# Performance work log

Hardware: AMD Instinct MI355X
Metric: run time of the kernel (lower is better)

## Reference

```python
import jax, jax.numpy as jnp
import numpy as np
import math

EMBED_DIM = 512
NUM_HEADS = 8
NUM_EXPERTS = 16
TOP_K = 8
B, T = 2, 1024


def setup_inputs() -> dict:
    key = jax.random.key(0)
    ks = jax.random.split(key, 16)
    d, E = EMBED_DIM, NUM_EXPERTS
    hdim = 4 * d  # expert hidden width
    s = 0.02
    inp = {
        "x": jax.random.normal(ks[0], (B, T, d), jnp.float32),
        # RMSNorm params (init ones, matching torch module)
        "g": jnp.ones((d,), jnp.float32),
        "b": jnp.ones((d,), jnp.float32),
        # attention
        "c_attn_w": jax.random.normal(ks[1], (d, 3 * d), jnp.float32) * s,
        "c_attn_b": jnp.zeros((3 * d,), jnp.float32),
        "alpha": jnp.ones((NUM_HEADS,), jnp.float32),
        "c_proj_w": jax.random.normal(ks[2], (d, d), jnp.float32) * s,
        "c_proj_b": jnp.zeros((d,), jnp.float32),
        # router
        "router_w": jax.random.normal(ks[3], (d, E), jnp.float32) * s,
        "router_b": jnp.zeros((E,), jnp.float32),
        # stacked expert params: Linear(d,4d) -> SwiGLU(4d,4d) -> Linear(4d,d)
        "w_in": jax.random.normal(ks[4], (E, d, hdim), jnp.float32) * s,
        "b_in": jnp.zeros((E, hdim), jnp.float32),
        "w1": jax.random.normal(ks[5], (E, hdim, 2 * hdim), jnp.float32) * s,
        "b1": jnp.zeros((E, 2 * hdim), jnp.float32),
        "w2": jax.random.normal(ks[6], (E, hdim, hdim), jnp.float32) * s,
        "b2": jnp.zeros((E, hdim), jnp.float32),
        "w_out": jax.random.normal(ks[7], (E, hdim, d), jnp.float32) * s,
        "b_out": jnp.zeros((E, d), jnp.float32),
    }
    return inp


def _block(x, g, b, c_attn_w, c_attn_b, alpha, c_proj_w, c_proj_b,
           router_w, router_b, w_in, b_in, w1, b1, w2, b2, w_out, b_out):
    Bb, Tt, C = x.shape
    H = alpha.shape[0]
    hd = C // H
    E = router_b.shape[0]

    # RMSNorm (note: additive b, per original module)
    rms = jnp.sqrt(jnp.mean(x * x, axis=-1, keepdims=True) + 1e-6)
    xn = (x / rms) * g + b

    # QK-normalized causal attention
    qkv = xn @ c_attn_w + c_attn_b                      # [B,T,3C]
    q, k, v = jnp.split(qkv, 3, axis=-1)
    def heads(t):
        return t.reshape(Bb, Tt, H, hd).transpose(0, 2, 1, 3)  # [B,H,T,hd]
    q, k, v = heads(q), heads(k), heads(v)
    eps = 1e-5
    q_hat = q / (jnp.linalg.norm(q, axis=-1, keepdims=True) + eps)
    k_hat = k / (jnp.linalg.norm(k, axis=-1, keepdims=True) + eps)
    factor = (alpha * math.sqrt(hd)).reshape(1, H, 1, 1)
    q_scaled = q_hat * factor
    # SDPA default scale = 1/sqrt(head_dim)
    scores = jnp.einsum("bhqd,bhkd->bhqk", q_scaled, k_hat) / math.sqrt(hd)
    causal = jnp.tril(jnp.ones((Tt, Tt), bool))
    scores = jnp.where(causal, scores, -jnp.inf)
    att = jax.nn.softmax(scores, axis=-1)
    y = jnp.einsum("bhqk,bhkd->bhqd", att, v)
    y = y.transpose(0, 2, 1, 3).reshape(Bb, Tt, C)
    y = y @ c_proj_w + c_proj_b
    x = x + y

    # Router + top-8 normalized gates
    routes = jax.nn.softmax(x @ router_w + router_b, axis=-1)  # [B,T,E]
    probs, idx = jax.lax.top_k(routes, TOP_K)
    probs = probs / jnp.sum(probs, axis=-1, keepdims=True)
    # combine weights per expert: [B,T,E]
    gates = jnp.sum(jax.nn.one_hot(idx, E, dtype=x.dtype) * probs[..., None], axis=2)

    # Dense expert evaluation (faithful math: unselected tokens get zero gate)
    N = Bb * Tt
    xf = x.reshape(N, C)
    gf = gates.reshape(N, E)
    h = jnp.einsum("nd,edf->enf", xf, w_in) + b_in[:, None, :]      # [E,N,4d]
    c = jnp.einsum("enf,efg->eng", h, w1) + b1[:, None, :]          # [E,N,8d]
    a, bb2 = jnp.split(c, 2, axis=-1)
    s = (bb2 * jax.nn.sigmoid(bb2)) * a                              # SwiGLU
    o = jnp.einsum("enf,efg->eng", s, w2) + b2[:, None, :]          # [E,N,4d]
    eo = jnp.einsum("enf,efd->end", o, w_out) + b_out[:, None, :]   # [E,N,d]
    moe = jnp.einsum("end,ne->nd", eo, gf).reshape(Bb, Tt, C)
    return x + moe


def reference(x, g, b, c_attn_w, c_attn_b, alpha, c_proj_w, c_proj_b,
              router_w, router_b, w_in, b_in, w1, b1, w2, b2, w_out, b_out):
    return _block(x, g, b, c_attn_w, c_attn_b, alpha, c_proj_w, c_proj_b,
                  router_w, router_b, w_in, b_in, w1, b1, w2, b2, w_out, b_out)
```

## Files before the change

kernel.cpp:

```cpp
#include <hip/hip_runtime.h>
#include <stdint.h>

#define DEVI __device__ __forceinline__
#define FENCE() asm volatile("" ::: "memory")

typedef short short8 __attribute__((ext_vector_type(8)));
typedef short short4v __attribute__((ext_vector_type(4)));
typedef float f32x4 __attribute__((ext_vector_type(4)));

DEVI float bf2f(unsigned short s){ union{unsigned u; float f;} x; x.u = ((unsigned)s)<<16; return x.f; }
DEVI unsigned short f2bf(float f){ union{float f; unsigned u;} x; x.f=f; unsigned r = x.u + 0x7fff + ((x.u>>16)&1); return (unsigned short)(r>>16); }

DEVI void gload_lds16(const void* g, void* l){
  __builtin_amdgcn_global_load_lds((const __attribute__((address_space(1))) unsigned int*)g,
                                   (__attribute__((address_space(3))) unsigned int*)l, 16, 0, 0);
}

__global__ __launch_bounds__(256)
void transpose_cvt(const float* __restrict__ in, unsigned short* __restrict__ out, int K, int N)
{
  __shared__ float tile[32][33];
  size_t zoff = (size_t)blockIdx.z * K * N;
  const float* src = in + zoff;
  unsigned short* dst = out + zoff;
  int kb = blockIdx.y*32, nb = blockIdx.x*32;
  int t = threadIdx.x;
  int tr = t>>3, tc = (t&7)*4;
  float4 v = *(const float4*)(src + (size_t)(kb+tr)*N + nb + tc);
  tile[tr][tc+0]=v.x; tile[tr][tc+1]=v.y; tile[tr][tc+2]=v.z; tile[tr][tc+3]=v.w;
  __syncthreads();
  short4v ov;
  ov[0] = (short)f2bf(tile[tc+0][tr]);
  ov[1] = (short)f2bf(tile[tc+1][tr]);
  ov[2] = (short)f2bf(tile[tc+2][tr]);
  ov[3] = (short)f2bf(tile[tc+3][tr]);
  *(short4v*)(dst + (size_t)(nb+tr)*K + kb + tc) = ov;
}

__global__ __launch_bounds__(256)
void transpose_cvt_w1(const float* __restrict__ w1, unsigned short* __restrict__ outp)
{
  __shared__ float tile[32][33];
  int e = blockIdx.z;
  const float* src = w1 + (size_t)e*2048*4096;
  unsigned short* dst = outp + (size_t)e*4096*2048;
  int np0 = blockIdx.x*32;
  int k0 = blockIdx.y*32;
  int g = np0 >> 5;
  int t = threadIdx.x;
  int tr = t>>3, tc = (t&7)*4;
  int srccol = (tc < 16) ? (g*16 + tc) : (2048 + g*16 + (tc-16));
  float4 v = *(const float4*)(src + (size_t)(k0+tr)*4096 + srccol);
  tile[tr][tc+0]=v.x; tile[tr][tc+1]=v.y; tile[tr][tc+2]=v.z; tile[tr][tc+3]=v.w;
  __syncthreads();
  short4v ov;
  ov[0] = (short)f2bf(tile[tc+0][tr]);
  ov[1] = (short)f2bf(tile[tc+1][tr]);
  ov[2] = (short)f2bf(tile[tc+2][tr]);
  ov[3] = (short)f2bf(tile[tc+3][tr]);
  *(short4v*)(dst + (size_t)(np0+tr)*2048 + k0 + tc) = ov;
}

__global__ __launch_bounds__(256)
void rmsnorm_k(const float* __restrict__ x, const float* __restrict__ gw,
               const float* __restrict__ bw, unsigned short* __restrict__ xn)
{
  int row = blockIdx.x*4 + (threadIdx.x>>6);
  int lane = threadIdx.x & 63;
  const float* xr = x + (size_t)row*512 + lane*8;
  float4 a = *(const float4*)xr;
  float4 c = *(const float4*)(xr+4);
  float ss = a.x*a.x+a.y*a.y+a.z*a.z+a.w*a.w + c.x*c.x+c.y*c.y+c.z*c.z+c.w*c.w;
  #pragma unroll
  for (int m=1;m<64;m<<=1) ss += __shfl_xor(ss, m);
  float inv = 1.0f / sqrtf(ss*(1.f/512.f) + 1e-6f);
  const float* gr = gw + lane*8; const float* br = bw + lane*8;
  float4 g0=*(const float4*)gr, g1=*(const float4*)(gr+4);
  float4 b0=*(const float4*)br, b1=*(const float4*)(br+4);
  short8 o;
  o[0]=(short)f2bf(a.x*inv*g0.x + b0.x);
  o[1]=(short)f2bf(a.y*inv*g0.y + b0.y);
  o[2]=(short)f2bf(a.z*inv*g0.z + b0.z);
  o[3]=(short)f2bf(a.w*inv*g0.w + b0.w);
  o[4]=(short)f2bf(c.x*inv*g1.x + b1.x);
  o[5]=(short)f2bf(c.y*inv*g1.y + b1.y);
  o[6]=(short)f2bf(c.z*inv*g1.z + b1.z);
  o[7]=(short)f2bf(c.w*inv*g1.w + b1.w);
  *(short8*)(xn + (size_t)row*512 + lane*8) = o;
}

template<int EPI>
__global__ __launch_bounds__(512, 2)
void gemm3(const unsigned short* __restrict__ A, const unsigned short* __restrict__ B,
           const float* __restrict__ bias,
           float* __restrict__ Cf, unsigned short* __restrict__ Ch,
           int M, int N, int K,
           const int* __restrict__ off, long long strideBz, long long strideBiasz)
{
  __shared__ char smem[147456];
  int nbx = gridDim.x, nby = gridDim.y;
  int pl = nbx*nby;
  int lin = ((int)blockIdx.z*nby + (int)blockIdx.y)*nbx + (int)blockIdx.x;
  int nwg = pl*(int)gridDim.z;
  int cpx = nwg >> 3;
  int swz = (lin & 7)*cpx + (lin >> 3);
  int z  = swz / pl; int rxy = swz - z*pl;
  int by = rxy / nbx; int bx = rxy - by*nbx;

  int rowbase = 0, Mz = M;
  if (off){ rowbase = off[z]; Mz = off[z+1] - rowbase; }
  int row0 = by * 256;
  if (row0 >= Mz) return;
  int col0 = bx * 128;
  const unsigned short* Ab = A + (size_t)(rowbase + row0) * K;
  const unsigned short* Bb = B + (size_t)z * strideBz + (size_t)col0 * K;
  const float* biasz = bias + (size_t)z * strideBiasz;

  int tid = threadIdx.x;
  int lane = tid & 63, w = tid >> 6;
  int lrow = lane & 15, lg = lane >> 4;
  int wr = w >> 1, wc = w & 1;

  f32x4 acc[4][4];
  #pragma unroll
  for (int i=0;i<4;i++){
    #pragma unroll
    for (int j=0;j<4;j++) acc[i][j] = f32x4{0.f,0.f,0.f,0.f};
  }

  int nkt = K >> 6;

  auto stage = [&](int kt2, int part){
    if (kt2 >= nkt) return;
    char* sA = smem + (kt2 % 3) * 49152;
    char* sB = sA + 32768;
    int k0 = kt2 << 6;
    #pragma unroll
    for (int i=0;i<2;i++){
      int s = (part*2 + i)*512 + tid;
      int r = s >> 3, kb = (s & 7) ^ (r & 7);
      gload_lds16(Ab + (size_t)r*K + k0 + kb*8, sA + s*16);
    }
    {
      int s = part*512 + tid;
      int r = s >> 3, kb = (s & 7) ^ (r & 7);
      gload_lds16(Bb + (size_t)r*K + k0 + kb*8, sB + s*16);
    }
  };

  stage(0,0); stage(0,1); stage(1,0); stage(1,1);
  asm volatile("s_waitcnt vmcnt(6)" ::: "memory");
  __builtin_amdgcn_s_barrier();
  FENCE();

  for (int kt = 0; kt < nkt; kt++){
    char* sA = smem + (kt % 3) * 49152;
    char* sB = sA + 32768;
    short8 bfr[4][2], afr[4][2];
    #pragma unroll
    for (int n=0;n<4;n++){
      int ct = wc*64 + n*16 + lrow;
      #pragma unroll
      for (int kk=0;kk<2;kk++){
        int kbb = lg + kk*4;
        bfr[n][kk] = *(const short8*)(sB + ct*128 + ((kbb ^ (ct&7))<<4));
      }
    }
    #pragma unroll
    for (int m=0;m<2;m++){
      int rt = wr*64 + m*16 + lrow;
      #pragma unroll
      for (int kk=0;kk<2;kk++){
        int kbb = lg + kk*4;
        afr[m][kk] = *(const short8*)(sA + rt*128 + ((kbb ^ (rt&7))<<4));
      }
    }
    stage(kt+2, 0);
    FENCE(); __builtin_amdgcn_s_barrier(); FENCE();
    __builtin_amdgcn_s_setprio(1);
    #pragma unroll
    for (int m=0;m<2;m++){
      #pragma unroll
      for (int n=0;n<4;n++){
        #pragma unroll
        for (int kk=0;kk<2;kk++)
          acc[m][n] = __builtin_amdgcn_mfma_f32_16x16x32_bf16(afr[m][kk], bfr[n][kk], acc[m][n], 0,0,0);
      }
    }
    __builtin_amdgcn_s_setprio(0);
    FENCE(); __builtin_amdgcn_s_barrier(); FENCE();
    #pragma unroll
    for (int m=2;m<4;m++){
      int rt = wr*64 + m*16 + lrow;
      #pragma unroll
      for (int kk=0;kk<2;kk++){
        int kbb = lg + kk*4;
        afr[m][kk] = *(const short8*)(sA + rt*128 + ((kbb ^ (rt&7))<<4));
      }
    }
    stage(kt+2, 1);
    FENCE(); __builtin_amdgcn_s_barrier(); FENCE();
    __builtin_amdgcn_s_setprio(1);
    #pragma unroll
    for (int m=2;m<4;m++){
      #pragma unroll
      for (int n=0;n<4;n++){
        #pragma unroll
        for (int kk=0;kk<2;kk++)
          acc[m][n] = __builtin_amdgcn_mfma_f32_16x16x32_bf16(afr[m][kk], bfr[n][kk], acc[m][n], 0,0,0);
      }
    }
    __builtin_amdgcn_s_setprio(0);
    if (kt + 2 < nkt) { asm volatile("s_waitcnt vmcnt(6)" ::: "memory"); }
    else              { asm volatile("s_waitcnt vmcnt(0)" ::: "memory"); }
    FENCE(); __builtin_amdgcn_s_barrier(); FENCE();
  }

  #pragma unroll
  for (int m=0;m<4;m++){
    int rloc = wr*64 + m*16 + lg*4;
    #pragma unroll
    for (int j=0;j<4;j++){
      int row = row0 + rloc + j;
      if (row < Mz){
        size_t rg = (size_t)(rowbase + row);
        if constexpr (EPI == 2){
          #pragma unroll
          for (int nf=0;nf<4;nf+=2){
            int pcol = col0 + wc*64 + nf*16;
            int scol = ((pcol>>5)<<4) + lrow;
            float av = acc[m][nf][j]   + biasz[scol];
            float gv = acc[m][nf+1][j] + biasz[2048 + scol];
            float sg = gv / (1.f + __expf(-gv));
            Ch[rg*2048 + scol] = f2bf(av * sg);
          }
        } else {
          #pragma unroll
          for (int n=0;n<4;n++){
            int col = col0 + wc*64 + n*16 + lrow;
            float v = acc[m][n][j] + biasz[col];
            size_t idx = rg * N + col;
            if constexpr (EPI == 0) Cf[idx] = v;
            else                    Ch[idx] = f2bf(v);
          }
        }
      }
    }
  }
}

__global__ __launch_bounds__(256)
void gemm_proj(const unsigned short* __restrict__ A, const unsigned short* __restrict__ B,
               const float* __restrict__ bias,
               float* __restrict__ Cf, unsigned short* __restrict__ Ch,
               const float* __restrict__ resid, int M, int N, int K)
{
  __shared__ char smem[32768];
  char* smA = smem; char* smB = smem + 16384;
  int row0 = blockIdx.y * 128;
  int col0 = blockIdx.x * 128;
  int t = threadIdx.x, w = t>>6, lane = t&63;
  int lrow = lane&15, lg = lane>>4;
  int wr = w>>1, wc = w&1;

  f32x4 acc[4][4];
  #pragma unroll
  for (int i=0;i<4;i++){
    #pragma unroll
    for (int j=0;j<4;j++) acc[i][j] = f32x4{0.f,0.f,0.f,0.f};
  }
  const size_t Abase = (size_t)row0 * K;
  const size_t Bbase = (size_t)col0 * K;
  int nkt = K >> 6;
  for (int kt=0; kt<nkt; kt++){
    __syncthreads();
    int k0 = kt*64;
    #pragma unroll
    for (int i=0;i<4;i++){
      int s = (i*4 + w)*64 + lane;
      int r = s>>3;
      int kb = (s&7) ^ (r&7);
      gload_lds16(A + Abase + (size_t)r*K + k0 + kb*8, smA + (size_t)(i*4+w)*1024);
      gload_lds16(B + Bbase + (size_t)r*K + k0 + kb*8, smB + (size_t)(i*4+w)*1024);
    }
    __syncthreads();
    #pragma unroll
    for (int ks=0; ks<2; ks++){
      short8 af[4], bf[4];
      int kbb = lg + ks*4;
      #pragma unroll
      for (int m=0;m<4;m++){
        int rt = wr*64 + m*16 + lrow;
        af[m] = *(const short8*)(smA + rt*128 + ((kbb ^ (rt&7))<<4));
      }
      #pragma unroll
      for (int n=0;n<4;n++){
        int rt = wc*64 + n*16 + lrow;
        bf[n] = *(const short8*)(smB + rt*128 + ((kbb ^ (rt&7))<<4));
      }
      #pragma unroll
      for (int m=0;m<4;m++){
        #pragma unroll
        for (int n=0;n<4;n++)
          acc[m][n] = __builtin_amdgcn_mfma_f32_16x16x32_bf16(af[m], bf[n], acc[m][n], 0,0,0);
      }
    }
  }
  #pragma unroll
  for (int m=0;m<4;m++){
    int rloc = wr*64 + m*16 + lg*4;
    #pragma unroll
    for (int j=0;j<4;j++){
      int row = row0 + rloc + j;
      size_t rg = (size_t)row;
      #pragma unroll
      for (int n=0;n<4;n++){
        int col = col0 + wc*64 + n*16 + lrow;
        float v = acc[m][n][j] + bias[col];
        size_t idx = rg * N + col;
        v += resid[idx];
        Cf[idx] = v;
        Ch[idx] = f2bf(v);
      }
    }
  }
}

__global__ __launch_bounds__(256)
void prep_qkv(const float* __restrict__ qkv, const float* __restrict__ alpha,
              unsigned short* __restrict__ q_s, unsigned short* __restrict__ k_hat,
              unsigned short* __restrict__ v_t)
{
  int idx = blockIdx.x*4 + (threadIdx.x>>6);
  int lane = threadIdx.x & 63;
  int h = idx & 7, bt = idx >> 3;
  size_t base = (size_t)bt*1536 + h*64 + lane;
  float qv = qkv[base], kv = qkv[base+512], vv = qkv[base+1024];
  float qs2 = qv*qv, ks2 = kv*kv;
  #pragma unroll
  for (int m=1;m<64;m<<=1){ qs2 += __shfl_xor(qs2, m); ks2 += __shfl_xor(ks2, m); }
  float qh = qv / (sqrtf(qs2) + 1e-5f) * alpha[h];
  float kh = kv / (sqrtf(ks2) + 1e-5f);
  int b = bt >> 10, tt = bt & 1023;
  size_t hb = ((size_t)(b*8+h))*1024*64;
  q_s[hb + (size_t)tt*64 + lane] = f2bf(qh);
  k_hat[hb + (size_t)tt*64 + lane] = f2bf(kh);
  v_t[((size_t)(b*8+h)*64 + lane)*1024 + tt] = f2bf(vv);
}

__global__ __launch_bounds__(256)
void attn_k(const unsigned short* __restrict__ q_s, const unsigned short* __restrict__ k_hat,
            const unsigned short* __restrict__ v_t, unsigned short* __restrict__ y)
{
  __shared__ char sm[51200];
  char* smK = sm + 18432;
  char* smV = sm + 34816;
  int qt = blockIdx.x, bh = blockIdx.y;
  int b = bh>>3, h = bh&7;
  int t = threadIdx.x, w = t>>6, lane = t&63;
  int lrow = lane&15, lg = lane>>4;
  int q0 = qt*64;
  const size_t hQK = (size_t)bh*1024*64;
  const size_t hV  = (size_t)bh*64*1024;

  #pragma unroll
  for (int i=0;i<2;i++){
    int si = i*256 + t;
    int r = si>>3, kb = (si&7)^(r&7);
    gload_lds16(q_s + hQK + (size_t)(q0+r)*64 + kb*8, sm + (size_t)si*16);
  }
  __syncthreads();
  short8 qf[2];
  #pragma unroll
  for (int ks=0;ks<2;ks++){
    int rt = w*16 + lrow;
    int kbb = lg + ks*4;
    qf[ks] = *(const short8*)(sm + rt*128 + ((kbb^(rt&7))<<4));
  }
  f32x4 oacc[4];
  #pragma unroll
  for (int j=0;j<4;j++) oacc[j] = f32x4{0.f,0.f,0.f,0.f};
  float mrun[4], lrun[4];
  #pragma unroll
  for (int j=0;j<4;j++){ mrun[j] = -1e30f; lrun[j] = 0.f; }
  char* Pw = sm + w*2304;

  int ktmax = (q0 + 63) >> 7;
  for (int kt=0; kt<=ktmax; kt++){
    __syncthreads();
    int t0 = kt*128;
    #pragma unroll
    for (int i=0;i<4;i++){
      int s = (i*4+w)*64 + lane;
      int r = s>>3, kb = (s&7)^(r&7);
      gload_lds16(k_hat + hQK + (size_t)(t0+r)*64 + kb*8, smK + (size_t)(i*4+w)*1024);
    }
    #pragma unroll
    for (int i=0;i<4;i++){
      int s = (i*4+w)*64 + lane;
      int d = s>>4, kb2 = s&15;
      int kb = kb2 ^ (d&7);
      gload_lds16(v_t + hV + (size_t)d*1024 + t0 + kb*8, smV + (size_t)(i*4+w)*1024);
    }
    __syncthreads();

    f32x4 sacc[8];
    #pragma unroll
    for (int j=0;j<8;j++) sacc[j] = f32x4{0.f,0.f,0.f,0.f};
    #pragma unroll
    for (int ks=0;ks<2;ks++){
      short8 kf[8];
      int kbb = lg + ks*4;
      #pragma unroll
      for (int nf=0;nf<8;nf++){
        int rt = nf*16+lrow;
        kf[nf] = *(const short8*)(smK + rt*128 + ((kbb^(rt&7))<<4));
      }
      #pragma unroll
      for (int nf=0;nf<8;nf++)
        sacc[nf] = __builtin_amdgcn_mfma_f32_16x16x32_bf16(qf[ks], kf[nf], sacc[nf], 0,0,0);
    }
    if (kt == ktmax){
      #pragma unroll
      for (int nf=0;nf<8;nf++){
        #pragma unroll
        for (int j=0;j<4;j++){
          int qi = q0 + w*16 + lg*4 + j;
          int ki = t0 + nf*16 + lrow;
          if (ki > qi) sacc[nf][j] = -1e30f;
        }
      }
    }
    #pragma unroll
    for (int j=0;j<4;j++){
      float mx = sacc[0][j];
      #pragma unroll
      for (int nf=1;nf<8;nf++) mx = fmaxf(mx, sacc[nf][j]);
      #pragma unroll
      for (int m=1;m<16;m<<=1) mx = fmaxf(mx, __shfl_xor(mx, m));
      float mnew = fmaxf(mrun[j], mx);
      float sc = __expf(mrun[j] - mnew);
      float rs = 0.f;
      #pragma unroll
      for (int nf=0;nf<8;nf++){
        float p = __expf(sacc[nf][j] - mnew);
        sacc[nf][j] = p; rs += p;
      }
      #pragma unroll
      for (int m=1;m<16;m<<=1) rs += __shfl_xor(rs, m);
      lrun[j] = lrun[j]*sc + rs;
      mrun[j] = mnew;
      #pragma unroll
      for (int n2=0;n2<4;n2++) oacc[n2][j] *= sc;
    }
    #pragma unroll
    for (int half=0; half<2; half++){
      #pragma unroll
      for (int nfh=0;nfh<4;nfh++){
        int nf = half*4 + nfh;
        #pragma unroll
        for (int j=0;j<4;j++){
          int row = lg*4 + j;
          int col = nfh*16 + lrow;
          *(unsigned short*)(Pw + (row*72 + col)*2) = f2bf(sacc[nf][j]);
        }
      }
      #pragma unroll
      for (int k2=0;k2<2;k2++){
        int ks2 = half*2 + k2;
        short8 pf, vf[4];
        pf = *(const short8*)(Pw + lrow*144 + lg*16 + k2*64);
        #pragma unroll
        for (int n2=0;n2<4;n2++){
          int d = n2*16+lrow;
          int kbb2 = lg + ks2*4;
          vf[n2] = *(const short8*)(smV + d*256 + ((kbb2^(d&7))<<4));
        }
        #pragma unroll
        for (int n2=0;n2<4;n2++)
          oacc[n2] = __builtin_amdgcn_mfma_f32_16x16x32_bf16(pf, vf[n2], oacc[n2], 0,0,0);
      }
    }
  }
  #pragma unroll
  for (int n2=0;n2<4;n2++){
    #pragma unroll
    for (int j=0;j<4;j++){
      float v = oacc[n2][j] / lrun[j];
      int qi = q0 + w*16 + lg*4 + j;
      int d = n2*16 + lrow;
      y[((size_t)(b*1024+qi))*512 + h*64 + d] = f2bf(v);
    }
  }
}

__global__ __launch_bounds__(256)
void router_topk(const float* __restrict__ x2f, const float* __restrict__ rw,
                 const float* __restrict__ rb, float* __restrict__ gates)
{
  int tkn = blockIdx.x*4 + (threadIdx.x>>6);
  int lane = threadIdx.x & 63;
  int e = lane & 15, p = lane >> 4;
  const float* xr = x2f + (size_t)tkn*512;
  float part = 0.f;
  for (int d = p*128; d < p*128+128; d++)
    part += xr[d] * rw[d*16 + e];
  part += __shfl_xor(part, 16);
  part += __shfl_xor(part, 32);
  float logit = part + rb[e];
  float mx = logit;
  #pragma unroll
  for (int m=1;m<16;m<<=1) mx = fmaxf(mx, __shfl_xor(mx, m));
  float ex = __expf(logit - mx);
  float sm = ex;
  #pragma unroll
  for (int m=1;m<16;m<<=1) sm += __shfl_xor(sm, m);
  float prob = ex / sm;
  bool taken = false;
  float ssum = 0.f;
  #pragma unroll
  for (int r=0;r<8;r++){
    float cv = taken ? -1.f : prob;
    int ci = e;
    #pragma unroll
    for (int m=1;m<16;m<<=1){
      float ov = __shfl_xor(cv, m);
      int oi = __shfl_xor(ci, m);
      if (ov > cv || (ov == cv && oi < ci)){ cv = ov; ci = oi; }
    }
    if (e == ci) taken = true;
    ssum += cv;
  }
  if (lane < 16)
    gates[(size_t)tkn*16 + e] = taken ? prob / ssum : 0.f;
}

__global__ void listbuild(const float* __restrict__ gates, int* __restrict__ list,
                          int* __restrict__ slot, int* __restrict__ cnt)
{
  int e = blockIdx.x;
  int tid = threadIdx.x, w = tid>>6, lane = tid&63;
  __shared__ int sbase;
  __shared__ int wsum[4];
  if (tid==0) sbase = 0;
  __syncthreads();
  for (int c=0;c<8;c++){
    int tk = c*256 + tid;
    bool flag = gates[(size_t)tk*16 + e] > 0.f;
    unsigned long long bal = __ballot(flag);
    if (lane==0) wsum[w] = (int)__popcll(bal);
    __syncthreads();
    int wpref = 0;
    for (int i=0;i<w;i++) wpref += wsum[i];
    int tot = wsum[0]+wsum[1]+wsum[2]+wsum[3];
    int lpref = (int)__popcll(bal & ((1ull<<lane)-1ull));
    if (flag){
      int pos = sbase + wpref + lpref;
      list[e*2048 + pos] = tk;
      slot[(size_t)tk*16 + e] = pos;
    }
    __syncthreads();
    if (tid==0) sbase += tot;
    __syncthreads();
  }
  if (tid==0) cnt[e] = sbase;
}

__global__ void prefix_off(const int* __restrict__ cnt, int* __restrict__ off){
  if (threadIdx.x==0 && blockIdx.x==0){
    int a=0;
    for (int e=0;e<16;e++){ off[e]=a; a+=cnt[e]; }
    off[16]=a;
  }
}

__global__ __launch_bounds__(256)
void gather_rows(const unsigned short* __restrict__ x2h, const int* __restrict__ list,
                 const int* __restrict__ cnt, const int* __restrict__ off,
                 unsigned short* __restrict__ xe)
{
  int e = blockIdx.y;
  int s = blockIdx.x*4 + (threadIdx.x>>6);
  if (s >= cnt[e]) return;
  int lane = threadIdx.x & 63;
  int tk = list[e*2048 + s];
  *(short8*)(xe + ((size_t)(off[e]+s))*512 + lane*8) =
      *(const short8*)(x2h + (size_t)tk*512 + lane*8);
}

__global__ __launch_bounds__(256)
void combine_k(const float* __restrict__ x2f, const unsigned short* __restrict__ eo,
               const float* __restrict__ gates, const int* __restrict__ slot,
               const int* __restrict__ off, float* __restrict__ out)
{
  int tkn = blockIdx.x;
  __shared__ float gs[16];
  __shared__ int rws[16];
  int tid = threadIdx.x;
  if (tid < 16){
    float g = gates[(size_t)tkn*16 + tid];
    gs[tid] = g;
    rws[tid] = (g > 0.f) ? (off[tid] + slot[(size_t)tkn*16 + tid]) : 0;
  }
  __syncthreads();
  for (int d = tid; d < 512; d += 256){
    float v = x2f[(size_t)tkn*512 + d];
    #pragma unroll
    for (int e=0;e<16;e++){
      float g = gs[e];
      if (g > 0.f) v += g * bf2f(eo[(size_t)rws[e]*512 + d]);
    }
    out[(size_t)tkn*512 + d] = v;
  }
}

extern "C" void kernel_launch(void* const* d_in, const int* in_sizes, int n_in,
                              void* d_out, int out_size, void* d_ws, size_t ws_size,
                              hipStream_t stream) {
  (void)in_sizes; (void)n_in; (void)out_size; (void)ws_size;
  const float* x    = (const float*)d_in[0];
  const float* gw   = (const float*)d_in[1];
  const float* bw   = (const float*)d_in[2];
  const float* caw  = (const float*)d_in[3];
  const float* cab  = (const float*)d_in[4];
  const float* alpha= (const float*)d_in[5];
  const float* cpw  = (const float*)d_in[6];
  const float* cpb  = (const float*)d_in[7];
  const float* rw   = (const float*)d_in[8];
  const float* rb   = (const float*)d_in[9];
  const float* w_in = (const float*)d_in[10];
  const float* b_in = (const float*)d_in[11];
  const float* w1   = (const float*)d_in[12];
  const float* b1   = (const float*)d_in[13];
  const float* w2   = (const float*)d_in[14];
  const float* b2   = (const float*)d_in[15];
  const float* w_out= (const float*)d_in[16];
  const float* b_out= (const float*)d_in[17];

  char* ws = (char*)d_ws;
  size_t o = 0;
  auto alloc = [&](size_t bytes)->char*{
    char* p = ws + o;
    o += (bytes + 255) & ~(size_t)255;
    return p;
  };
  const size_t PADROWS = 16896;
  unsigned short* wT_attn = (unsigned short*)alloc(1536ull*512*2);
  unsigned short* wT_proj = (unsigned short*)alloc(512ull*512*2);
  unsigned short* wT_in   = (unsigned short*)alloc(16ull*2048*512*2);
  unsigned short* wT1p    = (unsigned short*)alloc(16ull*4096*2048*2);
  unsigned short* wT_2    = (unsigned short*)alloc(16ull*2048*2048*2);
  unsigned short* wT_out  = (unsigned short*)alloc(16ull*512*2048*2);
  unsigned short* xn      = (unsigned short*)alloc(2048ull*512*2);
  float*          qkv     = (float*)alloc(2048ull*1536*4);
  unsigned short* q_s     = (unsigned short*)alloc(2048ull*512*2);
  unsigned short* k_hat   = (unsigned short*)alloc(2048ull*512*2);
  unsigned short* v_t     = (unsigned short*)alloc(2048ull*512*2);
  unsigned short* ybuf    = (unsigned short*)alloc(2048ull*512*2);
  float*          x2f     = (float*)alloc(2048ull*512*4);
  unsigned short* x2h     = (unsigned short*)alloc(2048ull*512*2);
  float*          gates   = (float*)alloc(2048ull*16*4);
  int*            slot    = (int*)alloc(2048ull*16*4);
  int*            list    = (int*)alloc(16ull*2048*4);
  int*            cnt     = (int*)alloc(64);
  int*            off     = (int*)alloc(256);
  unsigned short* xe      = (unsigned short*)alloc(PADROWS*512*2);
  unsigned short* hbuf    = (unsigned short*)alloc(PADROWS*2048*2);
  unsigned short* sbuf    = (unsigned short*)alloc(PADROWS*2048*2);
  unsigned short* eobuf   = xe;
  unsigned short* obuf    = hbuf;

  dim3 blk(256);
  dim3 blk5(512);
  transpose_cvt<<<dim3(1536/32, 512/32, 1), blk, 0, stream>>>(caw, wT_attn, 512, 1536);
  transpose_cvt<<<dim3(512/32, 512/32, 1), blk, 0, stream>>>(cpw, wT_proj, 512, 512);
  transpose_cvt<<<dim3(2048/32, 512/32, 16), blk, 0, stream>>>(w_in, wT_in, 512, 2048);
  transpose_cvt_w1<<<dim3(4096/32, 2048/32, 16), blk, 0, stream>>>(w1, wT1p);
  transpose_cvt<<<dim3(2048/32, 2048/32, 16), blk, 0, stream>>>(w2, wT_2, 2048, 2048);
  transpose_cvt<<<dim3(512/32, 2048/32, 16), blk, 0, stream>>>(w_out, wT_out, 2048, 512);

  rmsnorm_k<<<512, blk, 0, stream>>>(x, gw, bw, xn);
  gemm3<0><<<dim3(12, 8, 1), blk5, 0, stream>>>(xn, wT_attn, cab, qkv, nullptr,
                                                2048, 1536, 512, nullptr, 0, 0);
  prep_qkv<<<4096, blk, 0, stream>>>(qkv, alpha, q_s, k_hat, v_t);
  attn_k<<<dim3(16,16), blk, 0, stream>>>(q_s, k_hat, v_t, ybuf);
  gemm_proj<<<dim3(4,16,1), blk, 0, stream>>>(ybuf, wT_proj, cpb, x2f, x2h, x, 2048, 512, 512);
  router_topk<<<512, blk, 0, stream>>>(x2f, rw, rb, gates);
  listbuild<<<16, blk, 0, stream>>>(gates, list, slot, cnt);
  prefix_off<<<1, 64, 0, stream>>>(cnt, off);
  gather_rows<<<dim3(512,16), blk, 0, stream>>>(x2h, list, cnt, off, xe);

  gemm3<1><<<dim3(16,8,16), blk5, 0, stream>>>(xe, wT_in, b_in, nullptr, hbuf,
                                               0, 2048, 512, off, 2048ll*512, 2048);
  gemm3<2><<<dim3(32,8,16), blk5, 0, stream>>>(hbuf, wT1p, b1, nullptr, sbuf,
                                               0, 4096, 2048, off, 4096ll*2048, 4096);
  gemm3<1><<<dim3(16,8,16), blk5, 0, stream>>>(sbuf, wT_2, b2, nullptr, obuf,
                                               0, 2048, 2048, off, 2048ll*2048, 2048);
  gemm3<1><<<dim3(4,8,16), blk5, 0, stream>>>(obuf, wT_out, b_out, nullptr, eobuf,
                                              0, 512, 2048, off, 512ll*2048, 512);
  combine_k<<<2048, blk, 0, stream>>>(x2f, eobuf, gates, slot, off, (float*)d_out);
}
```

Measured before the change: 1.187 ms.

## Enlarge GEMM tiles to 256x256 with double-buffered LDS and quad-phased MFMA

Replaces the 256x128 triple-buffered GEMM with a 256x256 tile per workgroup. It uses a 2x4 wave layout with 128 accumulator fragments per wave, double-buffered LDS split into four quarter-stages, and compute interleaved in four phases with explicit lgkmcnt waits. It also drops the XCD-aware block swizzle. The larger tile raises arithmetic intensity and halves the number of workgroups, at the cost of higher register pressure, fewer blocks for load balance on the ragged per-expert row counts, and lost L2 locality from the removed swizzle.

New measurement: 1.109 ms. 1.07x faster.

```diff
diff --git a/kernel.cpp b/kernel.cpp
--- a/kernel.cpp
+++ b/kernel.cpp
@@ -3,6 +3,7 @@
 
 #define DEVI __device__ __forceinline__
 #define FENCE() asm volatile("" ::: "memory")
+#define BAR() do{ FENCE(); __builtin_amdgcn_s_barrier(); FENCE(); }while(0)
 
 typedef short short8 __attribute__((ext_vector_type(8)));
 typedef short short4v __attribute__((ext_vector_type(4)));
@@ -89,29 +90,50 @@
   *(short8*)(xn + (size_t)row*512 + lane*8) = o;
 }
 
+#define READ_AFR(Q) do{ \
+  _Pragma("unroll") \
+  for (int m2=0;m2<2;m2++){ \
+    int rt = wm*128 + ((Q)*2+m2)*16 + lrow; \
+    _Pragma("unroll") \
+    for (int kk=0;kk<2;kk++) \
+      afr[m2][kk] = *(const short8*)(sA + rt*128 + (((lg+kk*4)^(rt&7))<<4)); \
+  } \
+}while(0)
+
+#define QUADP(Q) do{ \
+  __builtin_amdgcn_s_setprio(1); \
+  _Pragma("unroll") \
+  for (int m2=0;m2<2;m2++){ \
+    _Pragma("unroll") \
+    for (int n=0;n<4;n++){ \
+      _Pragma("unroll") \
+      for (int kk=0;kk<2;kk++) \
+        acc[(Q)*2+m2][n] = __builtin_amdgcn_mfma_f32_16x16x32_bf16(afr[m2][kk], bfr[n][kk], acc[(Q)*2+m2][n], 0,0,0); \
+    } \
+  } \
+  __builtin_amdgcn_s_setprio(0); \
+}while(0)
+
+#define LGKM0() do{ \
+  asm volatile("s_waitcnt lgkmcnt(0)" ::: "memory"); \
+  __builtin_amdgcn_sched_barrier(0); \
+}while(0)
+
 template<int EPI>
 __global__ __launch_bounds__(512, 2)
-void gemm3(const unsigned short* __restrict__ A, const unsigned short* __restrict__ B,
+void gemmT(const unsigned short* __restrict__ A, const unsigned short* __restrict__ B,
            const float* __restrict__ bias,
            float* __restrict__ Cf, unsigned short* __restrict__ Ch,
            int M, int N, int K,
            const int* __restrict__ off, long long strideBz, long long strideBiasz)
 {
-  __shared__ char smem[147456];
-  int nbx = gridDim.x, nby = gridDim.y;
-  int pl = nbx*nby;
-  int lin = ((int)blockIdx.z*nby + (int)blockIdx.y)*nbx + (int)blockIdx.x;
-  int nwg = pl*(int)gridDim.z;
-  int cpx = nwg >> 3;
-  int swz = (lin & 7)*cpx + (lin >> 3);
-  int z  = swz / pl; int rxy = swz - z*pl;
-  int by = rxy / nbx; int bx = rxy - by*nbx;
-
+  __shared__ char smem[131072];
+  int z = blockIdx.z;
   int rowbase = 0, Mz = M;
   if (off){ rowbase = off[z]; Mz = off[z+1] - rowbase; }
-  int row0 = by * 256;
+  int row0 = blockIdx.y * 256;
   if (row0 >= Mz) return;
-  int col0 = bx * 128;
+  int col0 = blockIdx.x * 256;
   const unsigned short* Ab = A + (size_t)(rowbase + row0) * K;
   const unsigned short* Bb = B + (size_t)z * strideBz + (size_t)col0 * K;
   const float* biasz = bias + (size_t)z * strideBiasz;
@@ -119,115 +141,80 @@
   int tid = threadIdx.x;
   int lane = tid & 63, w = tid >> 6;
   int lrow = lane & 15, lg = lane >> 4;
-  int wr = w >> 1, wc = w & 1;
-
-  f32x4 acc[4][4];
-  #pragma unroll
-  for (int i=0;i<4;i++){
+  int wm = w >> 2, wn = w & 3;
+
+  f32x4 acc[8][4];
+  #pragma unroll
+  for (int i=0;i<8;i++){
     #pragma unroll
     for (int j=0;j<4;j++) acc[i][j] = f32x4{0.f,0.f,0.f,0.f};
   }
-
   int nkt = K >> 6;
-
-  auto stage = [&](int kt2, int part){
+  auto stage = [&](int kt2, int H){
     if (kt2 >= nkt) return;
-    char* sA = smem + (kt2 % 3) * 49152;
+    char* sl = smem + (kt2 & 1) * 65536 + H * 16384;
+    int k0 = kt2 << 6;
+    const unsigned short* src = (H < 2) ? Ab : Bb;
+    int rbase = (H & 1) * 128;
+    #pragma unroll
+    for (int i=0;i<2;i++){
+      int si = i*512 + tid;
+      int r = si >> 3, kb = (si & 7) ^ (r & 7);
+      gload_lds16(src + (size_t)(rbase + r)*K + k0 + kb*8, sl + si*16);
+    }
+  };
+  stage(0,0); stage(0,1); stage(0,2); stage(0,3);
+  stage(1,2); stage(1,3);
+  asm volatile("s_waitcnt vmcnt(4)" ::: "memory");
+  BAR();
+  for (int kt = 0; kt < nkt; kt++){
+    char* sA = smem + (kt & 1) * 65536;
     char* sB = sA + 32768;
-    int k0 = kt2 << 6;
-    #pragma unroll
-    for (int i=0;i<2;i++){
-      int s = (part*2 + i)*512 + tid;
-      int r = s >> 3, kb = (s & 7) ^ (r & 7);
-      gload_lds16(Ab + (size_t)r*K + k0 + kb*8, sA + s*16);
-    }
-    {
-      int s = part*512 + tid;
-      int r = s >> 3, kb = (s & 7) ^ (r & 7);
-      gload_lds16(Bb + (size_t)r*K + k0 + kb*8, sB + s*16);
-    }
-  };
-
-  stage(0,0); stage(0,1); stage(1,0); stage(1,1);
-  asm volatile("s_waitcnt vmcnt(6)" ::: "memory");
-  __builtin_amdgcn_s_barrier();
-  FENCE();
-
-  for (int kt = 0; kt < nkt; kt++){
-    char* sA = smem + (kt % 3) * 49152;
-    char* sB = sA + 32768;
-    short8 bfr[4][2], afr[4][2];
+    short8 bfr[4][2], afr[2][2];
     #pragma unroll
     for (int n=0;n<4;n++){
-      int ct = wc*64 + n*16 + lrow;
-      #pragma unroll
-      for (int kk=0;kk<2;kk++){
-        int kbb = lg + kk*4;
-        bfr[n][kk] = *(const short8*)(sB + ct*128 + ((kbb ^ (ct&7))<<4));
-      }
-    }
-    #pragma unroll
-    for (int m=0;m<2;m++){
-      int rt = wr*64 + m*16 + lrow;
-      #pragma unroll
-      for (int kk=0;kk<2;kk++){
-        int kbb = lg + kk*4;
-        afr[m][kk] = *(const short8*)(sA + rt*128 + ((kbb ^ (rt&7))<<4));
-      }
-    }
-    stage(kt+2, 0);
-    FENCE(); __builtin_amdgcn_s_barrier(); FENCE();
-    __builtin_amdgcn_s_setprio(1);
-    #pragma unroll
-    for (int m=0;m<2;m++){
-      #pragma unroll
-      for (int n=0;n<4;n++){
-        #pragma unroll
-        for (int kk=0;kk<2;kk++)
-          acc[m][n] = __builtin_amdgcn_mfma_f32_16x16x32_bf16(afr[m][kk], bfr[n][kk], acc[m][n], 0,0,0);
-      }
-    }
-    __builtin_amdgcn_s_setprio(0);
-    FENCE(); __builtin_amdgcn_s_barrier(); FENCE();
-    #pragma unroll
-    for (int m=2;m<4;m++){
-      int rt = wr*64 + m*16 + lrow;
-      #pragma unroll
-      for (int kk=0;kk<2;kk++){
-        int kbb = lg + kk*4;
-        afr[m][kk] = *(const short8*)(sA + rt*128 + ((kbb ^ (rt&7))<<4));
-      }
-    }
-    stage(kt+2, 1);
-    FENCE(); __builtin_amdgcn_s_barrier(); FENCE();
-    __builtin_amdgcn_s_setprio(1);
-    #pragma unroll
-    for (int m=2;m<4;m++){
-      #pragma unroll
-      for (int n=0;n<4;n++){
-        #pragma unroll
-        for (int kk=0;kk<2;kk++)
-          acc[m][n] = __builtin_amdgcn_mfma_f32_16x16x32_bf16(afr[m][kk], bfr[n][kk], acc[m][n], 0,0,0);
-      }
-    }
-    __builtin_amdgcn_s_setprio(0);
-    if (kt + 2 < nkt) { asm volatile("s_waitcnt vmcnt(6)" ::: "memory"); }
+      int ct = wn*64 + n*16 + lrow;
+      #pragma unroll
+      for (int kk=0;kk<2;kk++)
+        bfr[n][kk] = *(const short8*)(sB + ct*128 + (((lg+kk*4)^(ct&7))<<4));
+    }
+    READ_AFR(0);
+    stage(kt+1, 0); stage(kt+1, 1);
+    BAR();
+    LGKM0();
+    QUADP(0);
+    BAR();
+    READ_AFR(1);
+    stage(kt+2, 2);
+    BAR();
+    LGKM0();
+    QUADP(1);
+    BAR();
+    READ_AFR(2);
+    stage(kt+2, 3);
+    BAR();
+    LGKM0();
+    QUADP(2);
+    BAR();
+    READ_AFR(3);
+    if (kt + 2 < nkt) { asm volatile("s_waitcnt vmcnt(4)" ::: "memory"); }
     else              { asm volatile("s_waitcnt vmcnt(0)" ::: "memory"); }
-    FENCE(); __builtin_amdgcn_s_barrier(); FENCE();
-  }
-
-  #pragma unroll
-  for (int m=0;m<4;m++){
-    int rloc = wr*64 + m*16 + lg*4;
+    BAR();
+    LGKM0();
+    QUADP(3);
+    BAR();
+  }
+  #pragma unroll
+  for (int m=0;m<8;m++){
     #pragma unroll
     for (int j=0;j<4;j++){
-      int row = row0 + rloc + j;
+      int row = row0 + wm*128 + m*16 + lg*4 + j;
       if (row < Mz){
         size_t rg = (size_t)(rowbase + row);
         if constexpr (EPI == 2){
           #pragma unroll
           for (int nf=0;nf<4;nf+=2){
-            int pcol = col0 + wc*64 + nf*16;
+            int pcol = col0 + wn*64 + nf*16;
             int scol = ((pcol>>5)<<4) + lrow;
             float av = acc[m][nf][j]   + biasz[scol];
             float gv = acc[m][nf+1][j] + biasz[2048 + scol];
@@ -237,7 +224,7 @@
         } else {
           #pragma unroll
           for (int n=0;n<4;n++){
-            int col = col0 + wc*64 + n*16 + lrow;
+            int col = col0 + wn*64 + n*16 + lrow;
             float v = acc[m][n][j] + biasz[col];
             size_t idx = rg * N + col;
             if constexpr (EPI == 0) Cf[idx] = v;
@@ -680,8 +667,8 @@
   transpose_cvt<<<dim3(512/32, 2048/32, 16), blk, 0, stream>>>(w_out, wT_out, 2048, 512);
 
   rmsnorm_k<<<512, blk, 0, stream>>>(x, gw, bw, xn);
-  gemm3<0><<<dim3(12, 8, 1), blk5, 0, stream>>>(xn, wT_attn, cab, qkv, nullptr,
-                                                2048, 1536, 512, nullptr, 0, 0);
+  gemmT<0><<<dim3(6, 8, 1), blk5, 0, stream>>>(xn, wT_attn, cab, qkv, nullptr,
+                                               2048, 1536, 512, nullptr, 0, 0);
   prep_qkv<<<4096, blk, 0, stream>>>(qkv, alpha, q_s, k_hat, v_t);
   attn_k<<<dim3(16,16), blk, 0, stream>>>(q_s, k_hat, v_t, ybuf);
   gemm_proj<<<dim3(4,16,1), blk, 0, stream>>>(ybuf, wT_proj, cpb, x2f, x2h, x, 2048, 512, 512);
@@ -690,13 +677,13 @@
   prefix_off<<<1, 64, 0, stream>>>(cnt, off);
   gather_rows<<<dim3(512,16), blk, 0, stream>>>(x2h, list, cnt, off, xe);
 
-  gemm3<1><<<dim3(16,8,16), blk5, 0, stream>>>(xe, wT_in, b_in, nullptr, hbuf,
-                                               0, 2048, 512, off, 2048ll*512, 2048);
-  gemm3<2><<<dim3(32,8,16), blk5, 0, stream>>>(hbuf, wT1p, b1, nullptr, sbuf,
+  gemmT<1><<<dim3(8,8,16), blk5, 0, stream>>>(xe, wT_in, b_in, nullptr, hbuf,
+                                              0, 2048, 512, off, 2048ll*512, 2048);
+  gemmT<2><<<dim3(16,8,16), blk5, 0, stream>>>(hbuf, wT1p, b1, nullptr, sbuf,
                                                0, 4096, 2048, off, 4096ll*2048, 4096);
-  gemm3<1><<<dim3(16,8,16), blk5, 0, stream>>>(sbuf, wT_2, b2, nullptr, obuf,
-                                               0, 2048, 2048, off, 2048ll*2048, 2048);
-  gemm3<1><<<dim3(4,8,16), blk5, 0, stream>>>(obuf, wT_out, b_out, nullptr, eobuf,
+  gemmT<1><<<dim3(8,8,16), blk5, 0, stream>>>(sbuf, wT_2, b2, nullptr, obuf,
+                                              0, 2048, 2048, off, 2048ll*2048, 2048);
+  gemmT<1><<<dim3(2,8,16), blk5, 0, stream>>>(obuf, wT_out, b_out, nullptr, eobuf,
                                               0, 512, 2048, off, 512ll*2048, 512);
   combine_k<<<2048, blk, 0, stream>>>(x2f, eobuf, gates, slot, off, (float*)d_out);
 }
```
